# Kernel optimization log

Measured on AMD Instinct MI355X. Metric: run time of the kernel, lower is better.

Reference implementation:

```python
import jax, jax.numpy as jnp
import numpy as np

N_NODES = 100000
N_EDGES = 1600000
D_FEAT = 128
EPS = 0.0

def setup_inputs() -> dict:
    key = jax.random.key(0)
    k1, k2, k3 = jax.random.split(key, 3)
    feat = jax.random.normal(k1, (N_NODES, D_FEAT), dtype=jnp.float32)
    src = jax.random.randint(k2, (N_EDGES,), 0, N_NODES, dtype=jnp.int32)
    dst = jax.random.randint(k3, (N_EDGES,), 0, N_NODES, dtype=jnp.int32)
    return {"feat": feat, "src": src, "dst": dst}

def reference(feat, src, dst):
    # copy_u: gather messages from edge sources; sum-reduce into destinations
    msgs = feat[src]                                   # [E, D]
    neigh = jax.ops.segment_sum(msgs, dst, num_segments=N_NODES)  # [N, D]
    # (1 + eps) * feat_dst + aggregated neighbors
    return (1.0 + EPS) * feat + neigh
```

## Files before the change

kernel.cpp:

```cpp
#include <hip/hip_runtime.h>

#define D_FEAT 128
#define CAP 64
#define NXCD 8
#define NCHUNK 768
typedef unsigned int uint32;


__global__ void k_zero(uint32* __restrict__ p, int n) {
    int stride = gridDim.x * blockDim.x;
    for (int i = blockIdx.x * blockDim.x + threadIdx.x; i < n; i += stride)
        p[i] = 0u;
}

__global__ void k_fill_xcd(const int* __restrict__ src, const int* __restrict__ dst,
                           uint32* __restrict__ cur, int* __restrict__ adj,
                           int e, int per, int rsize, int n_nodes) {
    int xcd   = blockIdx.x & (NXCD - 1);
    int chunk = blockIdx.x >> 3;
    int lo = xcd * rsize;
    int hi = min(lo + rsize, n_nodes);
    int e0 = chunk * per;
    int e1 = min(e0 + per, e);
    for (int i = e0 + threadIdx.x; i < e1; i += blockDim.x) {
        int d = dst[i];
        if (d >= lo && d < hi) {
            uint32 p = atomicAdd(&cur[d], 1u);
            if (p < CAP) adj[(size_t)d * CAP + p] = src[i];
        }
    }
}

__global__ void k_gather4(const float4* __restrict__ feat4,
                          const uint32* __restrict__ deg,
                          const int* __restrict__ adj,
                          float4* __restrict__ out4, int n_nodes) {
    int gtid = blockIdx.x * blockDim.x + threadIdx.x;
    int wave = gtid >> 6;
    int lane = gtid & 63;
    int half = lane >> 5;
    int l    = lane & 31;
    int node = wave * 2 + half;
    if (node >= n_nodes) return;
    float4 acc = feat4[(size_t)node * 32 + l];
    int cnt = min((int)deg[node], CAP);
    for (int b = 0; b < cnt; b += 32) {
        int m = min(32, cnt - b);
        int a = (l < m) ? adj[(size_t)node * CAP + b + l] : 0;
        for (int j = 0; j < m; ++j) {
            int s = __shfl(a, j, 32);
            float4 v = feat4[(size_t)s * 32 + l];
            acc.x += v.x; acc.y += v.y; acc.z += v.z; acc.w += v.w;
        }
    }
    out4[(size_t)node * 32 + l] = acc;
}

__global__ void k_fill_slack(const int* __restrict__ src, const int* __restrict__ dst,
                             uint32* __restrict__ cur, int* __restrict__ adj, int e) {
    int i = blockIdx.x * blockDim.x + threadIdx.x;
    if (i < e) {
        int d = dst[i];
        uint32 p = atomicAdd(&cur[d], 1u);
        if (p < CAP) adj[(size_t)d * CAP + p] = src[i];
    }
}


__global__ void k_hist(const int* __restrict__ dst, uint32* __restrict__ deg, int e) {
    int i = blockIdx.x * blockDim.x + threadIdx.x;
    if (i < e) atomicAdd(&deg[dst[i]], 1u);
}

__global__ void k_scan1(const uint32* __restrict__ deg, uint32* __restrict__ offs,
                        uint32* __restrict__ bsum, int n) {
    __shared__ uint32 lds[256];
    int t = threadIdx.x;
    int i0 = blockIdx.x * 1024 + t * 4;
    uint32 v[4];
    for (int k = 0; k < 4; ++k) { int i = i0 + k; v[k] = (i < n) ? deg[i] : 0u; }
    uint32 tsum = v[0] + v[1] + v[2] + v[3];
    lds[t] = tsum; __syncthreads();
    uint32 run = tsum;
    for (int off = 1; off < 256; off <<= 1) {
        uint32 add = (t >= off) ? lds[t - off] : 0u; __syncthreads();
        run += add; lds[t] = run; __syncthreads();
    }
    uint32 p = run - tsum;
    for (int k = 0; k < 4; ++k) { int i = i0 + k; if (i < n) offs[i] = p; p += v[k]; }
    if (t == 255) bsum[blockIdx.x] = run;
}

__global__ void k_scan2(uint32* __restrict__ bsum, int nb) {
    __shared__ uint32 lds[256];
    int t = threadIdx.x;
    uint32 v = (t < nb) ? bsum[t] : 0u;
    lds[t] = v; __syncthreads();
    uint32 run = v;
    for (int off = 1; off < 256; off <<= 1) {
        uint32 add = (t >= off) ? lds[t - off] : 0u; __syncthreads();
        run += add; lds[t] = run; __syncthreads();
    }
    if (t < nb) bsum[t] = run - v;
}

__global__ void k_scan3(uint32* __restrict__ offs, uint32* __restrict__ cur,
                        const uint32* __restrict__ bsum, int n) {
    int i0 = blockIdx.x * 1024 + threadIdx.x * 4;
    uint32 add = bsum[blockIdx.x];
    for (int k = 0; k < 4; ++k) {
        int i = i0 + k;
        if (i < n) { uint32 o = offs[i] + add; offs[i] = o; cur[i] = o; }
    }
}

__global__ void k_fill(const int* __restrict__ src, const int* __restrict__ dst,
                       uint32* __restrict__ cur, int* __restrict__ adj, int e) {
    int i = blockIdx.x * blockDim.x + threadIdx.x;
    if (i < e) {
        int d = dst[i];
        uint32 p = atomicAdd(&cur[d], 1u);
        adj[p] = src[i];
    }
}

__global__ void k_gather(const float2* __restrict__ feat2,
                         const uint32* __restrict__ offs,
                         const uint32* __restrict__ endp,
                         const int* __restrict__ adj,
                         float2* __restrict__ out2, int n_nodes) {
    int gtid = blockIdx.x * blockDim.x + threadIdx.x;
    int node = gtid >> 6;
    int lane = gtid & 63;
    if (node >= n_nodes) return;
    float2 acc = feat2[(size_t)node * 64 + lane];
    int e0 = (int)offs[node];
    int e1 = (int)endp[node];
    for (int b = e0; b < e1; b += 64) {
        int cnt = min(64, e1 - b);
        int a = (lane < cnt) ? adj[b + lane] : 0;
        for (int j = 0; j < cnt; ++j) {
            int s = __shfl(a, j);
            float2 v = feat2[(size_t)s * 64 + lane];
            acc.x += v.x; acc.y += v.y;
        }
    }
    out2[(size_t)node * 64 + lane] = acc;
}


__global__ void init_out_kernel(const float4* __restrict__ feat,
                                float4* __restrict__ out, int n4) {
    int stride = gridDim.x * blockDim.x;
    for (int i = blockIdx.x * blockDim.x + threadIdx.x; i < n4; i += stride)
        out[i] = feat[i];
}

__global__ void scatter_edges_kernel(const float* __restrict__ feat,
                                     const int* __restrict__ src,
                                     const int* __restrict__ dst,
                                     float* __restrict__ out, int n_edges) {
    long long stride = (long long)gridDim.x * blockDim.x;
    long long total  = (long long)n_edges * 32;
    for (long long gtid = (long long)blockIdx.x * blockDim.x + threadIdx.x;
         gtid < total; gtid += stride) {
        int edge = (int)(gtid >> 5);
        int lane = (int)(gtid & 31);
        int s = src[edge];
        int d = dst[edge];
        const float4 v =
            *reinterpret_cast<const float4*>(feat + (size_t)s * D_FEAT + lane * 4);
        float* op = out + (size_t)d * D_FEAT + lane * 4;
        unsafeAtomicAdd(op + 0, v.x);
        unsafeAtomicAdd(op + 1, v.y);
        unsafeAtomicAdd(op + 2, v.z);
        unsafeAtomicAdd(op + 3, v.w);
    }
}

extern "C" void kernel_launch(void* const* d_in, const int* in_sizes, int n_in,
                              void* d_out, int out_size, void* d_ws, size_t ws_size,
                              hipStream_t stream) {
    const float* feat = (const float*)d_in[0];
    const int*   src  = (const int*)d_in[1];
    const int*   dst  = (const int*)d_in[2];
    float*       out  = (float*)d_out;

    int n_feat  = in_sizes[0];
    int n_edges = in_sizes[1];
    int n_nodes = n_feat / D_FEAT;
    int blk = 256;

    size_t need0 = ((size_t)n_nodes * CAP + n_nodes) * sizeof(uint32);
    if (ws_size >= need0) {
        int*    adj = (int*)d_ws;
        uint32* cur = (uint32*)(adj + (size_t)n_nodes * CAP);

        k_zero<<<256, blk, 0, stream>>>(cur, n_nodes);

        int per   = (n_edges + NCHUNK - 1) / NCHUNK;
        int rsize = (n_nodes + NXCD - 1) / NXCD;
        k_fill_xcd<<<NXCD * NCHUNK, blk, 0, stream>>>(
            src, dst, cur, adj, n_edges, per, rsize, n_nodes);

        int nwaves = (n_nodes + 1) / 2;
        long long gthreads = (long long)nwaves * 64;
        k_gather4<<<(int)((gthreads + blk - 1) / blk), blk, 0, stream>>>(
            (const float4*)feat, cur, adj, (float4*)out, n_nodes);
        return;
    }

    int nb = (n_nodes + 1023) / 1024;
    size_t need1 = ((size_t)3 * n_nodes + 256 + (size_t)n_edges) * sizeof(uint32);
    if (ws_size >= need1 && nb <= 256) {
        uint32* deg  = (uint32*)d_ws;
        uint32* offs = deg  + n_nodes;
        uint32* cur  = offs + n_nodes;
        uint32* bsum = cur  + n_nodes;
        int*    adj  = (int*)(bsum + 256);

        k_zero <<<256, blk, 0, stream>>>(deg, n_nodes);
        k_hist <<<(n_edges + blk - 1) / blk, blk, 0, stream>>>(dst, deg, n_edges);
        k_scan1<<<nb, blk, 0, stream>>>(deg, offs, bsum, n_nodes);
        k_scan2<<<1, blk, 0, stream>>>(bsum, nb);
        k_scan3<<<nb, blk, 0, stream>>>(offs, cur, bsum, n_nodes);
        k_fill <<<(n_edges + blk - 1) / blk, blk, 0, stream>>>(src, dst, cur, adj, n_edges);

        long long gthreads = (long long)n_nodes * 64;
        k_gather<<<(int)((gthreads + blk - 1) / blk), blk, 0, stream>>>(
            (const float2*)feat, offs, cur, adj, (float2*)out, n_nodes);
        return;
    }

    int n4 = n_feat / 4;
    init_out_kernel<<<min((n4 + blk - 1) / blk, 2048), blk, 0, stream>>>(
        (const float4*)feat, (float4*)out, n4);
    long long total_threads = (long long)n_edges * 32;
    int grid_sc = (int)min((total_threads + blk - 1) / blk, (long long)8192);
    scatter_edges_kernel<<<grid_sc, blk, 0, stream>>>(feat, src, dst, out, n_edges);
}
```

Before: 283.3 us.

## Pre-bin edges by destination range before adjacency fill

Replaces the fill kernel, in which every block rescanned all edges and kept only its destination range, with a two-pass scheme. A binning kernel first partitions (src,dst) pairs into 8 destination-range buckets through LDS staging, writing them into the output buffer as scratch. A second kernel then fills the adjacency per bucket, so blockIdx low bits map each bucket to one XCD. This removes the 8x redundant reads of dst, at the cost of an extra write and read of the pair array plus shared-memory atomics.

```diff
diff --git a/kernel.cpp b/kernel.cpp
--- a/kernel.cpp
+++ b/kernel.cpp
@@ -2,8 +2,8 @@
 
 #define D_FEAT 128
 #define CAP 64
-#define NXCD 8
-#define NCHUNK 768
+#define NBKT 8
+#define BKT_DEPTH 384
 typedef unsigned int uint32;
 
 
@@ -13,21 +13,65 @@
         p[i] = 0u;
 }
 
-__global__ void k_fill_xcd(const int* __restrict__ src, const int* __restrict__ dst,
-                           uint32* __restrict__ cur, int* __restrict__ adj,
-                           int e, int per, int rsize, int n_nodes) {
-    int xcd   = blockIdx.x & (NXCD - 1);
-    int chunk = blockIdx.x >> 3;
-    int lo = xcd * rsize;
-    int hi = min(lo + rsize, n_nodes);
-    int e0 = chunk * per;
-    int e1 = min(e0 + per, e);
-    for (int i = e0 + threadIdx.x; i < e1; i += blockDim.x) {
-        int d = dst[i];
-        if (d >= lo && d < hi) {
-            uint32 p = atomicAdd(&cur[d], 1u);
-            if (p < CAP) adj[(size_t)d * CAP + p] = src[i];
-        }
+__global__ __launch_bounds__(1024) void k_bin(
+        const int* __restrict__ src, const int* __restrict__ dst,
+        int2* __restrict__ pairs, uint32* __restrict__ bcur,
+        int e, int rsize, int bcap) {
+    __shared__ int2   buf[NBKT][BKT_DEPTH];
+    __shared__ uint32 cnt[NBKT];
+    __shared__ uint32 base[NBKT];
+    int nt = blockDim.x;
+    for (int t0 = blockIdx.x * nt; t0 < e; t0 += gridDim.x * nt) {
+        if (threadIdx.x < NBKT) cnt[threadIdx.x] = 0u;
+        __syncthreads();
+        int i = t0 + threadIdx.x;
+        int flag = 0;
+        int2 pr;
+        int b = 0;
+        if (i < e) {
+            pr.x = src[i]; pr.y = dst[i];
+            b = pr.y / rsize; if (b >= NBKT) b = NBKT - 1;
+            uint32 p = atomicAdd(&cnt[b], 1u);
+            if (p < BKT_DEPTH) { buf[b][p] = pr; flag = 1; }
+            else flag = 2;
+        }
+        __syncthreads();
+        if (threadIdx.x < NBKT) {
+            uint32 c = min(cnt[threadIdx.x], (uint32)BKT_DEPTH);
+            base[threadIdx.x] = c ? atomicAdd(&bcur[threadIdx.x], c) : 0u;
+            cnt[threadIdx.x] = c;
+        }
+        __syncthreads();
+        for (int b2 = 0; b2 < NBKT; ++b2) {
+            uint32 c = cnt[b2];
+            for (uint32 k = threadIdx.x; k < c; k += nt) {
+                uint32 gp = base[b2] + k;
+                if (gp < (uint32)bcap) pairs[(size_t)b2 * bcap + gp] = buf[b2][k];
+            }
+        }
+        if (flag == 2) {
+            uint32 gp = atomicAdd(&bcur[b], 1u);
+            if (gp < (uint32)bcap) pairs[(size_t)b * bcap + gp] = pr;
+        }
+        __syncthreads();
+    }
+}
+
+__global__ void k_fill_b(const int2* __restrict__ pairs,
+                         const uint32* __restrict__ bcur,
+                         uint32* __restrict__ cur, int* __restrict__ adj,
+                         int bcap) {
+    int bkt    = blockIdx.x & (NBKT - 1);
+    int chunk  = blockIdx.x >> 3;
+    int nchunk = gridDim.x >> 3;
+    int cnt = (int)min(bcur[bkt], (uint32)bcap);
+    int per = (cnt + nchunk - 1) / nchunk;
+    int s0 = chunk * per;
+    int s1 = min(cnt, s0 + per);
+    for (int k = s0 + threadIdx.x; k < s1; k += blockDim.x) {
+        int2 pr = pairs[(size_t)bkt * bcap + k];
+        uint32 p = atomicAdd(&cur[pr.y], 1u);
+        if (p < CAP) adj[(size_t)pr.y * CAP + p] = pr.x;
     }
 }
 
@@ -56,16 +100,6 @@
     out4[(size_t)node * 32 + l] = acc;
 }
 
-__global__ void k_fill_slack(const int* __restrict__ src, const int* __restrict__ dst,
-                             uint32* __restrict__ cur, int* __restrict__ adj, int e) {
-    int i = blockIdx.x * blockDim.x + threadIdx.x;
-    if (i < e) {
-        int d = dst[i];
-        uint32 p = atomicAdd(&cur[d], 1u);
-        if (p < CAP) adj[(size_t)d * CAP + p] = src[i];
-    }
-}
-
 
 __global__ void k_hist(const int* __restrict__ dst, uint32* __restrict__ deg, int e) {
     int i = blockIdx.x * blockDim.x + threadIdx.x;
@@ -191,17 +225,22 @@
     int n_nodes = n_feat / D_FEAT;
     int blk = 256;
 
-    size_t need0 = ((size_t)n_nodes * CAP + n_nodes) * sizeof(uint32);
-    if (ws_size >= need0) {
-        int*    adj = (int*)d_ws;
-        uint32* cur = (uint32*)(adj + (size_t)n_nodes * CAP);
-
-        k_zero<<<256, blk, 0, stream>>>(cur, n_nodes);
-
-        int per   = (n_edges + NCHUNK - 1) / NCHUNK;
-        int rsize = (n_nodes + NXCD - 1) / NXCD;
-        k_fill_xcd<<<NXCD * NCHUNK, blk, 0, stream>>>(
-            src, dst, cur, adj, n_edges, per, rsize, n_nodes);
+    int rsize = (n_nodes + NBKT - 1) / NBKT;
+    int bcap  = n_edges / NBKT + 8192;
+    size_t need0 = ((size_t)n_nodes * CAP + n_nodes + NBKT) * sizeof(uint32);
+    size_t pairs_bytes = (size_t)NBKT * bcap * sizeof(int2);
+
+    if (ws_size >= need0 && pairs_bytes <= (size_t)out_size * sizeof(float)) {
+        int*    adj  = (int*)d_ws;
+        uint32* cur  = (uint32*)(adj + (size_t)n_nodes * CAP);
+        uint32* bcur = cur + n_nodes;
+        int2*   pairs = (int2*)d_out;
+
+        k_zero<<<256, blk, 0, stream>>>(cur, n_nodes + NBKT);
+
+        k_bin<<<256, 1024, 0, stream>>>(src, dst, pairs, bcur, n_edges, rsize, bcap);
+
+        k_fill_b<<<NBKT * 256, blk, 0, stream>>>(pairs, bcur, cur, adj, bcap);
 
         int nwaves = (n_nodes + 1) / 2;
         long long gthreads = (long long)nwaves * 64;
```

New measurement: 299.5 us. 5.7% more time.
